# Performance work log

Measured on AMD Instinct MI355X. Metric: run time of the kernel, lower is better.

The kernel has to match this reference:

```python
import jax, jax.numpy as jnp
import numpy as np

B, T, E = 512, 12, 1024   # batch, channels/seq, embed_dim
NH, HS = 8, 128           # num_heads, head_size (head_size=128 hard-coded in source)
H = NH * HS               # sLSTM hidden = 1024 (== E)


def _layer_norm(x, g, b, eps=1e-5):
    mu = x.mean(-1, keepdims=True)
    var = x.var(-1, keepdims=True)
    return (x - mu) * jax.lax.rsqrt(var + eps) * g + b


def _conv1d_same(x, w, b):
    # x: (B, C, L), w: (O, I, K) odd K, 'same' padding, stride 1
    k = w.shape[-1]
    p = (k - 1) // 2
    y = jax.lax.conv_general_dilated(x, w, (1,), [(p, p)],
                                     dimension_numbers=('NCH', 'OIH', 'NCH'))
    return y + b[None, :, None]


def setup_inputs():
    key = jax.random.key(0)
    ks = jax.random.split(key, 16)
    s = 0.02
    def nrm(k, shape, scale=s):
        return jax.random.normal(k, shape, jnp.float32) * scale
    return {
        'x': jax.random.normal(ks[0], (B, T, E), jnp.float32),
        'ln_g': jnp.ones((E,), jnp.float32), 'ln_b': jnp.zeros((E,), jnp.float32),
        'fc1_w': nrm(ks[1], (12, 12, 3)), 'fc1_b': jnp.zeros((12,), jnp.float32),
        'fc2_w': nrm(ks[2], (12, 12)), 'fc2_b': jnp.zeros((12,), jnp.float32),
        'conv1_w': nrm(ks[3], (48, 12, 3)), 'conv1_b': jnp.zeros((48,), jnp.float32),
        'conv2_w': nrm(ks[4], (12, 48, 3)), 'conv2_b': jnp.zeros((12,), jnp.float32),
        'xl_ln_g': jnp.ones((E,), jnp.float32), 'xl_ln_b': jnp.zeros((E,), jnp.float32),
        'Wg': nrm(ks[5], (E, 4 * H)), 'bg': jnp.zeros((4 * H,), jnp.float32),
        'Rg': nrm(ks[6], (NH, 4 * HS, HS)),
        'gn_g': jnp.ones((H,), jnp.float32), 'gn_b': jnp.zeros((H,), jnp.float32),
        'upl_w': nrm(ks[7], (H, H)), 'upl_b': jnp.zeros((H,), jnp.float32),
        'upr_w': nrm(ks[8], (H, H)), 'upr_b': jnp.zeros((H,), jnp.float32),
        'down_w': nrm(ks[9], (H, E)), 'down_b': jnp.zeros((E,), jnp.float32),
    }


def _slstm_block(x, xl_ln_g, xl_ln_b, Wg, bg, Rg, gn_g, gn_b,
                 upl_w, upl_b, upr_w, upr_b, down_w, down_b):
    # Stabilized multi-head sLSTM block: pre-LN -> sLSTM recurrence (exp i/f gates
    # with max-stabilizer m), per-head GroupNorm, gated up/down proj (proj_factor=1),
    # residual. Recurrent weights are block-diagonal per head (NH, 4*HS, HS).
    xn = _layer_norm(x, xl_ln_g, xl_ln_b)
    gx = jnp.einsum('bte,eg->btg', xn, Wg) + bg            # (B,T,4H) input gate pre-acts
    gx = jnp.swapaxes(gx, 0, 1)                            # (T,B,4H)

    def step(carry, g_t):
        h, c, n, m = carry                                 # each (B,NH,HS)
        rec = jnp.einsum('bnh,ngh->bng', h, Rg)            # (B,NH,4HS)
        g = g_t.reshape(g_t.shape[0], NH, 4 * HS) + rec
        z_, i_, f_, o_ = jnp.split(g, 4, axis=-1)
        z = jnp.tanh(z_)
        o = jax.nn.sigmoid(o_)
        m_new = jnp.maximum(f_ + m, i_)                    # log-space stabilizer
        i = jnp.exp(i_ - m_new)
        f = jnp.exp(f_ + m - m_new)
        c = f * c + i * z
        n = f * n + i
        h = o * (c / n)
        return (h, c, n, m_new), h

    zero = jnp.zeros((x.shape[0], NH, HS), x.dtype)
    _, hseq = jax.lax.scan(step, (zero, zero, zero, zero), gx)
    h = jnp.swapaxes(hseq, 0, 1)                           # (B,T,NH,HS)
    # GroupNorm(num_groups=NH) over each head's HS channels
    mu = h.mean(-1, keepdims=True)
    var = h.var(-1, keepdims=True)
    hn = (h - mu) * jax.lax.rsqrt(var + 1e-5)
    hn = hn.reshape(x.shape[0], x.shape[1], H) * gn_g + gn_b
    left = jax.nn.gelu(hn @ upl_w + upl_b, approximate=False)
    right = hn @ upr_w + upr_b
    return (left * right) @ down_w + down_b + x


def reference(x, ln_g, ln_b, fc1_w, fc1_b, fc2_w, fc2_b, conv1_w, conv1_b,
              conv2_w, conv2_b, xl_ln_g, xl_ln_b, Wg, bg, Rg, gn_g, gn_b,
              upl_w, upl_b, upr_w, upr_b, down_w, down_b):
    xn = _layer_norm(x, ln_g, ln_b)
    skip = xn
    xc = _conv1d_same(xn, fc1_w, fc1_b)                    # fc1: Conv1d(12,12,3,'same')
    x1 = jnp.einsum('bcl,oc->bol', xc, fc2_w) + fc2_b[None, :, None]  # fc2: 1x1 conv
    x1 = _slstm_block(x1, xl_ln_g, xl_ln_b, Wg, bg, Rg, gn_g, gn_b,
                      upl_w, upl_b, upr_w, upr_b, down_w, down_b)
    # dropout(0.2) is identity in eval mode
    y = jax.nn.silu(xc) * x1 + skip
    z = _conv1d_same(y, conv1_w, conv1_b)                  # 12 -> 48
    z = _layer_norm(jax.nn.gelu(z, approximate=False), ln_g, ln_b)
    z = _conv1d_same(z, conv2_w, conv2_b)                  # 48 -> 12
    return z + skip
```

## Files before the change

kernel.cpp:

```cpp
#include <hip/hip_runtime.h>
#include <math.h>


typedef short short8_t __attribute__((ext_vector_type(8)));
typedef float floatx4 __attribute__((ext_vector_type(4)));
typedef float float4_t __attribute__((ext_vector_type(4)));

typedef unsigned int u32;
typedef const __attribute__((address_space(1))) u32 gu32;
typedef __attribute__((address_space(3))) u32 lu32;

static __device__ __forceinline__ float b2f(unsigned short u) {
    unsigned v = ((unsigned)u) << 16;
    return __builtin_bit_cast(float, v);
}
static __device__ __forceinline__ unsigned short f2b(float f) {
    unsigned u = __builtin_bit_cast(unsigned, f);
    u += 0x7FFFu + ((u >> 16) & 1u);
    return (unsigned short)(u >> 16);
}
static __device__ __forceinline__ float gelu_exact(float x) {
    return 0.5f * x * (1.f + erff(x * 0.70710678118654752f));
}


__global__ __launch_bounds__(256) void transpose_bf16_k(
    const float* __restrict__ src, unsigned short* __restrict__ dst, int K, int N)
{
    __shared__ unsigned short tl[32][33];
    const int n0 = blockIdx.x * 32, k0 = blockIdx.y * 32;
    const int tx = threadIdx.x & 31, ty = threadIdx.x >> 5;
#pragma unroll
    for (int r = 0; r < 4; r++) {
        int k = ty + r * 8;
        tl[tx][k] = f2b(src[(size_t)(k0 + k) * N + n0 + tx]);
    }
    __syncthreads();
#pragma unroll
    for (int r = 0; r < 4; r++) {
        int n = ty * 4 + r;
        dst[(size_t)(n0 + n) * K + k0 + tx] = tl[n][tx];
    }
}

__global__ __launch_bounds__(256) void cat_bias_k(
    const float* __restrict__ a, const float* __restrict__ b, float* __restrict__ o)
{
    int gid = blockIdx.x * 256 + threadIdx.x;
    o[gid] = (gid < 1024) ? a[gid] : b[gid - 1024];
}


template <int BF16OUT>
__global__ __launch_bounds__(256) void ln_kernel(
    const float* __restrict__ in, const float* __restrict__ g,
    const float* __restrict__ be, void* __restrict__ outp)
{
    const int row = blockIdx.x;
    const float* xr = in + (size_t)row * 1024;
    const int t = threadIdx.x;
    float v[4];
    float s = 0.f, ss = 0.f;
#pragma unroll
    for (int u = 0; u < 4; u++) {
        float q = xr[t + u * 256];
        v[u] = q; s += q; ss += q * q;
    }
#pragma unroll
    for (int off = 32; off >= 1; off >>= 1) {
        s += __shfl_xor(s, off);
        ss += __shfl_xor(ss, off);
    }
    __shared__ float red[8];
    const int wv = t >> 6, la = t & 63;
    if (la == 0) { red[wv] = s; red[4 + wv] = ss; }
    __syncthreads();
    s = red[0] + red[1] + red[2] + red[3];
    ss = red[4] + red[5] + red[6] + red[7];
    float mu = s * (1.f / 1024.f);
    float var = ss * (1.f / 1024.f) - mu * mu;
    float rs = rsqrtf(var + 1e-5f);
#pragma unroll
    for (int u = 0; u < 4; u++) {
        int i = t + u * 256;
        float yv = (v[u] - mu) * rs * g[i] + be[i];
        if (BF16OUT)
            ((unsigned short*)outp)[(size_t)row * 1024 + i] = f2b(yv);
        else
            ((float*)outp)[(size_t)row * 1024 + i] = yv;
    }
}


__global__ __launch_bounds__(256) void fc_kernel(
    const float* __restrict__ xn,
    const float* __restrict__ w1, const float* __restrict__ b1,
    const float* __restrict__ w2, const float* __restrict__ b2,
    float* __restrict__ xc, float* __restrict__ x1)
{
    const int t = threadIdx.x;
    const int gid = blockIdx.x * 256 + t;
    const int b = gid >> 10, l = gid & 1023;
    const float* xb = xn + (size_t)b * 12288;
    float inm[12], in0[12], inp[12];
#pragma unroll
    for (int ci = 0; ci < 12; ci++) {
        in0[ci] = xb[ci * 1024 + l];
        inm[ci] = (l > 0) ? xb[ci * 1024 + l - 1] : 0.f;
        inp[ci] = (l < 1023) ? xb[ci * 1024 + l + 1] : 0.f;
    }
    float xcv[12];
#pragma unroll
    for (int o = 0; o < 12; o++) {
        float a = b1[o];
#pragma unroll
        for (int ci = 0; ci < 12; ci++) {
            const float* wp = w1 + o * 36 + ci * 3;
            a += inm[ci] * wp[0] + in0[ci] * wp[1] + inp[ci] * wp[2];
        }
        xcv[o] = a;
        xc[(size_t)b * 12288 + o * 1024 + l] = a;
    }
#pragma unroll
    for (int o = 0; o < 12; o++) {
        float a = b2[o];
#pragma unroll
        for (int ci = 0; ci < 12; ci++) a += xcv[ci] * w2[o * 12 + ci];
        x1[(size_t)b * 12288 + o * 1024 + l] = a;
    }
}


template <int MODE>
__global__ __launch_bounds__(256) void gemm_kernel(
    const unsigned short* __restrict__ A, const unsigned short* __restrict__ BT,
    const float* __restrict__ bias, void* __restrict__ out,
    int M, int N, int K,
    const float* __restrict__ xc, const float* __restrict__ x1,
    const float* __restrict__ skip)
{
    __shared__ __align__(16) unsigned short sA[128 * 32];
    __shared__ __align__(16) unsigned short sB[128 * 32];
    const int t = threadIdx.x;
    const int m0 = blockIdx.y * 128;
    const int n0 = blockIdx.x * 128;
    const int w = t >> 6;
    const int lane = t & 63;
    const int wr = (w >> 1) * 64;
    const int wc = (w & 1) * 64;
    const int lrow = lane & 15;
    const int quad = lane >> 4;
    const int row_l = t >> 2;
    const int cs = (t & 3) * 8;

    const unsigned short* gA0 = A + (size_t)(m0 + row_l) * K + cs;
    const unsigned short* gA1 = A + (size_t)(m0 + row_l + 64) * K + cs;
    const unsigned short* gB0 = BT + (size_t)(n0 + row_l) * K + cs;
    const unsigned short* gB1 = BT + (size_t)(n0 + row_l + 64) * K + cs;
    unsigned short* lA0 = sA + w * 512;
    unsigned short* lA1 = sA + 2048 + w * 512;
    unsigned short* lB0 = sB + w * 512;
    unsigned short* lB1 = sB + 2048 + w * 512;

    floatx4 acc[4][4];
#pragma unroll
    for (int i = 0; i < 4; i++)
#pragma unroll
        for (int j = 0; j < 4; j++) acc[i][j] = (floatx4)0.f;

    for (int k0 = 0; k0 < K; k0 += 32) {
        __syncthreads();
        __builtin_amdgcn_global_load_lds((gu32*)(gA0 + k0), (lu32*)lA0, 16, 0, 0);
        __builtin_amdgcn_global_load_lds((gu32*)(gA1 + k0), (lu32*)lA1, 16, 0, 0);
        __builtin_amdgcn_global_load_lds((gu32*)(gB0 + k0), (lu32*)lB0, 16, 0, 0);
        __builtin_amdgcn_global_load_lds((gu32*)(gB1 + k0), (lu32*)lB1, 16, 0, 0);
        __syncthreads();
        short8_t af[4], bfr[4];
#pragma unroll
        for (int i = 0; i < 4; i++) {
            af[i] = *(const short8_t*)(sA + (wr + i * 16 + lrow) * 32 + quad * 8);
            bfr[i] = *(const short8_t*)(sB + (wc + i * 16 + lrow) * 32 + quad * 8);
        }
#pragma unroll
        for (int i = 0; i < 4; i++)
#pragma unroll
            for (int j = 0; j < 4; j++)
                acc[i][j] = __builtin_amdgcn_mfma_f32_16x16x32_bf16(
                    af[i], bfr[j], acc[i][j], 0, 0, 0);
    }

#pragma unroll
    for (int i = 0; i < 4; i++) {
#pragma unroll
        for (int j = 0; j < 4; j++) {
#pragma unroll
            for (int r = 0; r < 4; r++) {
                const int gm = m0 + wr + i * 16 + quad * 4 + r;
                const int gn = n0 + wc + j * 16 + lrow;
                const size_t idx = (size_t)gm * N + gn;
                float v = acc[i][j][r] + bias[gn];
                if (MODE == 0) {
                    ((unsigned short*)out)[idx] = f2b(v);
                } else {
                    float xcv = xc[idx];
                    float sig = xcv / (1.f + __expf(-xcv));
                    ((float*)out)[idx] = sig * (v + x1[idx]) + skip[idx];
                }
            }
        }
    }
}


#define RECP 516
#define HBP  136

__global__ __launch_bounds__(1024, 4) void slstm_rec_kernel(
    const float* __restrict__ Rg,
    const unsigned short* __restrict__ gxb,
    const float* __restrict__ gn_g, const float* __restrict__ gn_b,
    unsigned short* __restrict__ hnb)
{
    __shared__ __align__(16) float sRec[16 * RECP];
    __shared__ __align__(16) unsigned short sHb[16 * HBP];
    const int head = blockIdx.x;
    const int b0 = blockIdx.y * 16;
    const int t = threadIdx.x;
    const int w = t >> 6;
    const int lane = t & 63;
    const int quad = lane >> 4;
    const int l16 = lane & 15;

    short8_t Bf[2][4];
    {
        const float* Rh = Rg + (size_t)head * 65536;
#pragma unroll
        for (int jt = 0; jt < 2; jt++)
#pragma unroll
            for (int kk = 0; kk < 4; kk++) {
                const float* src =
                    Rh + (size_t)(w * 32 + jt * 16 + l16) * 128 + kk * 32 + quad * 8;
                short8_t v;
#pragma unroll
                for (int j = 0; j < 8; j++) v[j] = (short)f2b(src[j]);
                Bf[jt][kk] = v;
            }
    }

    for (int i = t; i < 16 * HBP; i += 1024) sHb[i] = 0;

    const int la = lane;
    float c0 = 0.f, n0s = 0.f, m0 = 0.f;
    float c1 = 0.f, n1s = 0.f, m1 = 0.f;
    const float gg0 = gn_g[head * 128 + la];
    const float gg1 = gn_g[head * 128 + la + 64];
    const float gb0 = gn_b[head * 128 + la];
    const float gb1 = gn_b[head * 128 + la + 64];

    __syncthreads();

    for (int step = 0; step < 12; step++) {
        const unsigned short* gp =
            gxb + ((size_t)(b0 + w) * 12 + step) * 4096 + head * 512;
        float gz0 = b2f(gp[la]),       gz1 = b2f(gp[64 + la]);
        float gi0 = b2f(gp[128 + la]), gi1 = b2f(gp[192 + la]);
        float gf0 = b2f(gp[256 + la]), gf1 = b2f(gp[320 + la]);
        float go0 = b2f(gp[384 + la]), go1 = b2f(gp[448 + la]);

        short8_t Af[4];
#pragma unroll
        for (int kk = 0; kk < 4; kk++)
            Af[kk] = *(const short8_t*)(sHb + l16 * HBP + kk * 32 + quad * 8);
        floatx4 D0 = (floatx4)0.f, D1 = (floatx4)0.f;
#pragma unroll
        for (int kk = 0; kk < 4; kk++) {
            D0 = __builtin_amdgcn_mfma_f32_16x16x32_bf16(Af[kk], Bf[0][kk], D0, 0, 0, 0);
            D1 = __builtin_amdgcn_mfma_f32_16x16x32_bf16(Af[kk], Bf[1][kk], D1, 0, 0, 0);
        }
#pragma unroll
        for (int r = 0; r < 4; r++) {
            sRec[(quad * 4 + r) * RECP + w * 32 + l16] = D0[r];
            sRec[(quad * 4 + r) * RECP + w * 32 + 16 + l16] = D1[r];
        }
        __syncthreads();

        const float* rr = sRec + w * RECP;
        float zp0 = gz0 + rr[la],       zp1 = gz1 + rr[64 + la];
        float ip0 = gi0 + rr[128 + la], ip1 = gi1 + rr[192 + la];
        float fp0 = gf0 + rr[256 + la], fp1 = gf1 + rr[320 + la];
        float op0 = go0 + rr[384 + la], op1 = go1 + rr[448 + la];

        float e20 = __expf(2.f * zp0), e21 = __expf(2.f * zp1);
        float z0 = (e20 - 1.f) / (e20 + 1.f), z1 = (e21 - 1.f) / (e21 + 1.f);
        float o0 = 1.f / (1.f + __expf(-op0)), o1 = 1.f / (1.f + __expf(-op1));
        float mn0 = fmaxf(fp0 + m0, ip0), mn1 = fmaxf(fp1 + m1, ip1);
        float ie0 = __expf(ip0 - mn0), ie1 = __expf(ip1 - mn1);
        float fe0 = __expf(fp0 + m0 - mn0), fe1 = __expf(fp1 + m1 - mn1);
        c0 = fe0 * c0 + ie0 * z0;  c1 = fe1 * c1 + ie1 * z1;
        n0s = fe0 * n0s + ie0;     n1s = fe1 * n1s + ie1;
        m0 = mn0;                  m1 = mn1;
        float h0 = o0 * (c0 / n0s), h1 = o1 * (c1 / n1s);

        float s = h0 + h1, ss = h0 * h0 + h1 * h1;
#pragma unroll
        for (int off = 32; off >= 1; off >>= 1) {
            s += __shfl_xor(s, off);
            ss += __shfl_xor(ss, off);
        }
        float mu = s * (1.f / 128.f);
        float var = ss * (1.f / 128.f) - mu * mu;
        float rs = rsqrtf(var + 1e-5f);
        size_t base = ((size_t)(b0 + w) * 12 + step) * 1024 + head * 128;
        hnb[base + la] = f2b((h0 - mu) * rs * gg0 + gb0);
        hnb[base + la + 64] = f2b((h1 - mu) * rs * gg1 + gb1);

        sHb[w * HBP + la] = f2b(h0);
        sHb[w * HBP + la + 64] = f2b(h1);
        __syncthreads();
    }
}


__global__ __launch_bounds__(256) void gate_kernel(
    const unsigned short* __restrict__ lr, unsigned short* __restrict__ glr)
{
    size_t gid = (size_t)blockIdx.x * 256 + threadIdx.x;
    size_t m = gid >> 10;
    int j = (int)(gid & 1023);
    float lf = b2f(lr[m * 2048 + j]);
    float rt = b2f(lr[m * 2048 + 1024 + j]);
    glr[gid] = f2b(gelu_exact(lf) * rt);
}


__global__ __launch_bounds__(1024, 4) void tail_fused_kernel(
    const float* __restrict__ y, const float* __restrict__ skip,
    const float* __restrict__ w1, const float* __restrict__ b1,
    const float* __restrict__ w2, const float* __restrict__ b2,
    const float* __restrict__ lng, const float* __restrict__ lnb,
    float* __restrict__ out)
{
    __shared__ unsigned short sY[12][1032];
    __shared__ unsigned short sZ[48][1032];
    __shared__ float sLg[1024], sLb[1024];
    __shared__ float sMR[48][2];
    const int b = blockIdx.x;
    const int t = threadIdx.x;

    {
        const float* yb = y + (size_t)b * 12288;
#pragma unroll
        for (int r = 0; r < 12; r++) sY[r][t] = f2b(yb[r * 1024 + t]);
    }
    sLg[t] = lng[t];
    sLb[t] = lnb[t];
    __syncthreads();

    float vm[12], v0[12], vp[12];
#pragma unroll
    for (int ci = 0; ci < 12; ci++) {
        v0[ci] = b2f(sY[ci][t]);
        vm[ci] = (t > 0) ? b2f(sY[ci][t - 1]) : 0.f;
        vp[ci] = (t < 1023) ? b2f(sY[ci][t + 1]) : 0.f;
    }
    for (int o = 0; o < 48; o++) {
        const float* wp = w1 + o * 36;
        float a = b1[o];
#pragma unroll
        for (int ci = 0; ci < 12; ci++)
            a += vm[ci] * wp[ci * 3] + v0[ci] * wp[ci * 3 + 1] + vp[ci] * wp[ci * 3 + 2];
        sZ[o][t] = f2b(gelu_exact(a));
    }
    __syncthreads();

    {
        const int w = t >> 6, la = t & 63;
        for (int o = w * 3; o < w * 3 + 3; o++) {
            float s = 0.f, ss = 0.f;
#pragma unroll
            for (int u = 0; u < 16; u++) {
                float v = b2f(sZ[o][la + u * 64]);
                s += v; ss += v * v;
            }
#pragma unroll
            for (int off = 32; off >= 1; off >>= 1) {
                s += __shfl_xor(s, off);
                ss += __shfl_xor(ss, off);
            }
            if (la == 0) {
                float mu = s * (1.f / 1024.f);
                float var = ss * (1.f / 1024.f) - mu * mu;
                sMR[o][0] = mu;
                sMR[o][1] = rsqrtf(var + 1e-5f);
            }
        }
    }
    __syncthreads();

    float acc[12];
#pragma unroll
    for (int o = 0; o < 12; o++) acc[o] = b2[o];
    const float lg0 = sLg[t], lb0 = sLb[t];
    const float lgm = (t > 0) ? sLg[t - 1] : 0.f;
    const float lbm = (t > 0) ? sLb[t - 1] : 0.f;
    const float lgp = (t < 1023) ? sLg[t + 1] : 0.f;
    const float lbp = (t < 1023) ? sLb[t + 1] : 0.f;
    for (int ci = 0; ci < 48; ci++) {
        const float mu = sMR[ci][0], rs = sMR[ci][1];
        float znm = (t > 0) ? ((b2f(sZ[ci][t - 1]) - mu) * rs * lgm + lbm) : 0.f;
        float zn0 = (b2f(sZ[ci][t]) - mu) * rs * lg0 + lb0;
        float znp = (t < 1023) ? ((b2f(sZ[ci][t + 1]) - mu) * rs * lgp + lbp) : 0.f;
        const float* wp = w2 + ci * 3;
#pragma unroll
        for (int o = 0; o < 12; o++)
            acc[o] += znm * wp[o * 144] + zn0 * wp[o * 144 + 1] + znp * wp[o * 144 + 2];
    }
    const size_t base = (size_t)b * 12288 + t;
#pragma unroll
    for (int o = 0; o < 12; o++) {
        size_t idx = base + (size_t)o * 1024;
        out[idx] = acc[o] + skip[idx];
    }
}


extern "C" void kernel_launch(void* const* d_in, const int* in_sizes, int n_in,
                              void* d_out, int out_size, void* d_ws, size_t ws_size,
                              hipStream_t stream)
{
    (void)in_sizes; (void)n_in; (void)out_size; (void)ws_size;
    const float* x      = (const float*)d_in[0];
    const float* ln_g   = (const float*)d_in[1];
    const float* ln_b   = (const float*)d_in[2];
    const float* fc1_w  = (const float*)d_in[3];
    const float* fc1_b  = (const float*)d_in[4];
    const float* fc2_w  = (const float*)d_in[5];
    const float* fc2_b  = (const float*)d_in[6];
    const float* conv1_w= (const float*)d_in[7];
    const float* conv1_b= (const float*)d_in[8];
    const float* conv2_w= (const float*)d_in[9];
    const float* conv2_b= (const float*)d_in[10];
    const float* xl_g   = (const float*)d_in[11];
    const float* xl_b   = (const float*)d_in[12];
    const float* Wg     = (const float*)d_in[13];
    const float* bg     = (const float*)d_in[14];
    const float* Rg     = (const float*)d_in[15];
    const float* gn_g   = (const float*)d_in[16];
    const float* gn_b   = (const float*)d_in[17];
    const float* upl_w  = (const float*)d_in[18];
    const float* upl_b  = (const float*)d_in[19];
    const float* upr_w  = (const float*)d_in[20];
    const float* upr_b  = (const float*)d_in[21];
    const float* down_w = (const float*)d_in[22];
    const float* down_b = (const float*)d_in[23];

    char* ws = (char*)d_ws;
    size_t off = 0;
    auto alloc = [&](size_t bytes) -> char* {
        char* p = ws + off;
        off = (off + bytes + 255) & ~(size_t)255;
        return p;
    };
    float* xn            = (float*)alloc(25165824);
    float* xc            = (float*)alloc(25165824);
    float* x1            = (float*)alloc(25165824);
    unsigned short* xn2b = (unsigned short*)alloc(12582912);
    unsigned short* gxb  = (unsigned short*)alloc(50331648);
    unsigned short* hnb  = (unsigned short*)alloc(12582912);
    unsigned short* lrb  = (unsigned short*)alloc(25165824);
    unsigned short* glrb = (unsigned short*)alloc(12582912);
    float* yb            = (float*)alloc(25165824);
    unsigned short* WgT  = (unsigned short*)alloc(8388608);
    unsigned short* WupT = (unsigned short*)alloc(4194304);
    unsigned short* WdT  = (unsigned short*)alloc(2097152);
    float* bup           = (float*)alloc(8192);

    transpose_bf16_k<<<dim3(128, 32), 256, 0, stream>>>(Wg, WgT, 1024, 4096);
    transpose_bf16_k<<<dim3(32, 32), 256, 0, stream>>>(upl_w, WupT, 1024, 1024);
    transpose_bf16_k<<<dim3(32, 32), 256, 0, stream>>>(upr_w, WupT + 1024 * 1024, 1024, 1024);
    transpose_bf16_k<<<dim3(32, 32), 256, 0, stream>>>(down_w, WdT, 1024, 1024);
    cat_bias_k<<<8, 256, 0, stream>>>(upl_b, upr_b, bup);

    ln_kernel<0><<<6144, 256, 0, stream>>>(x, ln_g, ln_b, xn);
    fc_kernel<<<2048, 256, 0, stream>>>(xn, fc1_w, fc1_b, fc2_w, fc2_b, xc, x1);
    ln_kernel<1><<<6144, 256, 0, stream>>>(x1, xl_g, xl_b, xn2b);
    gemm_kernel<0><<<dim3(32, 48), 256, 0, stream>>>(
        xn2b, WgT, bg, gxb, 6144, 4096, 1024, nullptr, nullptr, nullptr);
    slstm_rec_kernel<<<dim3(8, 32), 1024, 0, stream>>>(Rg, gxb, gn_g, gn_b, hnb);
    gemm_kernel<0><<<dim3(16, 48), 256, 0, stream>>>(
        hnb, WupT, bup, lrb, 6144, 2048, 1024, nullptr, nullptr, nullptr);
    gate_kernel<<<24576, 256, 0, stream>>>(lrb, glrb);
    gemm_kernel<2><<<dim3(8, 48), 256, 0, stream>>>(
        glrb, WdT, down_b, yb, 6144, 1024, 1024, xc, x1, xn);
    tail_fused_kernel<<<512, 1024, 0, stream>>>(
        yb, xn, conv1_w, conv1_b, conv2_w, conv2_b, ln_g, ln_b, (float*)d_out);
}
```

Baseline: 482.4 us.

## Fuse frontend LN/conv/LN into one kernel and restructure tail conv kernel

Merges the first layernorm, the fc1/fc2 convolutions and the second layernorm into a single per-batch kernel that keeps the normalized input in shared memory, removing two launches and the intermediate global round trips. The tail kernel is rebuilt with 512 threads, each handling two positions, and processes the 48 conv1 channels in two halves of 24 so it needs less shared memory. Normalization is applied once in place in shared memory instead of per tap. Exact erf GELU in the tail is replaced with a tanh approximation, which changes numerics slightly. The fused frontend's 1024-thread blocks with 12 channels of state per thread may raise register pressure.

```diff
diff --git a/kernel.cpp b/kernel.cpp
--- a/kernel.cpp
+++ b/kernel.cpp
@@ -4,7 +4,7 @@
 
 typedef short short8_t __attribute__((ext_vector_type(8)));
 typedef float floatx4 __attribute__((ext_vector_type(4)));
-typedef float float4_t __attribute__((ext_vector_type(4)));
+typedef float float2_t __attribute__((ext_vector_type(2)));
 
 typedef unsigned int u32;
 typedef const __attribute__((address_space(1))) u32 gu32;
@@ -22,6 +22,13 @@
 static __device__ __forceinline__ float gelu_exact(float x) {
     return 0.5f * x * (1.f + erff(x * 0.70710678118654752f));
 }
+static __device__ __forceinline__ float gelu_fast(float x) {
+    float u = 0.7978845608f * x * (1.f + 0.044715f * x * x);
+    u = fminf(fmaxf(u, -9.f), 9.f);
+    float e = __expf(2.f * u);
+    float t = (e - 1.f) / (e + 1.f);
+    return 0.5f * x * (1.f + t);
+}
 
 
 __global__ __launch_bounds__(256) void transpose_bf16_k(
@@ -51,82 +58,109 @@
 }
 
 
-template <int BF16OUT>
-__global__ __launch_bounds__(256) void ln_kernel(
-    const float* __restrict__ in, const float* __restrict__ g,
-    const float* __restrict__ be, void* __restrict__ outp)
-{
-    const int row = blockIdx.x;
-    const float* xr = in + (size_t)row * 1024;
-    const int t = threadIdx.x;
-    float v[4];
-    float s = 0.f, ss = 0.f;
-#pragma unroll
-    for (int u = 0; u < 4; u++) {
-        float q = xr[t + u * 256];
-        v[u] = q; s += q; ss += q * q;
-    }
-#pragma unroll
-    for (int off = 32; off >= 1; off >>= 1) {
-        s += __shfl_xor(s, off);
-        ss += __shfl_xor(ss, off);
-    }
-    __shared__ float red[8];
-    const int wv = t >> 6, la = t & 63;
-    if (la == 0) { red[wv] = s; red[4 + wv] = ss; }
-    __syncthreads();
-    s = red[0] + red[1] + red[2] + red[3];
-    ss = red[4] + red[5] + red[6] + red[7];
-    float mu = s * (1.f / 1024.f);
-    float var = ss * (1.f / 1024.f) - mu * mu;
-    float rs = rsqrtf(var + 1e-5f);
-#pragma unroll
-    for (int u = 0; u < 4; u++) {
-        int i = t + u * 256;
-        float yv = (v[u] - mu) * rs * g[i] + be[i];
-        if (BF16OUT)
-            ((unsigned short*)outp)[(size_t)row * 1024 + i] = f2b(yv);
-        else
-            ((float*)outp)[(size_t)row * 1024 + i] = yv;
-    }
-}
-
-
-__global__ __launch_bounds__(256) void fc_kernel(
-    const float* __restrict__ xn,
+__global__ __launch_bounds__(1024, 4) void frontend_fused_kernel(
+    const float* __restrict__ x,
+    const float* __restrict__ ln_g, const float* __restrict__ ln_b,
     const float* __restrict__ w1, const float* __restrict__ b1,
     const float* __restrict__ w2, const float* __restrict__ b2,
-    float* __restrict__ xc, float* __restrict__ x1)
-{
+    const float* __restrict__ xl_g, const float* __restrict__ xl_b,
+    float* __restrict__ xn, float* __restrict__ xc, float* __restrict__ x1,
+    unsigned short* __restrict__ xn2b)
+{
+    __shared__ float sXn[12][1026];
+    __shared__ float sred[12][16][2];
+    __shared__ float sMR[12][2];
+    const int b = blockIdx.x;
     const int t = threadIdx.x;
-    const int gid = blockIdx.x * 256 + t;
-    const int b = gid >> 10, l = gid & 1023;
-    const float* xb = xn + (size_t)b * 12288;
-    float inm[12], in0[12], inp[12];
+    const int w = t >> 6, la = t & 63;
+    const size_t boff = (size_t)b * 12288;
+
+    float xv[12];
+#pragma unroll
+    for (int ci = 0; ci < 12; ci++) xv[ci] = x[boff + ci * 1024 + t];
+
 #pragma unroll
     for (int ci = 0; ci < 12; ci++) {
-        in0[ci] = xb[ci * 1024 + l];
-        inm[ci] = (l > 0) ? xb[ci * 1024 + l - 1] : 0.f;
-        inp[ci] = (l < 1023) ? xb[ci * 1024 + l + 1] : 0.f;
+        float s = xv[ci], ss = xv[ci] * xv[ci];
+#pragma unroll
+        for (int off = 32; off >= 1; off >>= 1) {
+            s += __shfl_xor(s, off); ss += __shfl_xor(ss, off);
+        }
+        if (la == 0) { sred[ci][w][0] = s; sred[ci][w][1] = ss; }
+    }
+    __syncthreads();
+    if (w < 12 && la == 0) {
+        float s = 0.f, ss = 0.f;
+        for (int u = 0; u < 16; u++) { s += sred[w][u][0]; ss += sred[w][u][1]; }
+        float mu = s * (1.f / 1024.f);
+        float var = ss * (1.f / 1024.f) - mu * mu;
+        sMR[w][0] = mu; sMR[w][1] = rsqrtf(var + 1e-5f);
+    }
+    __syncthreads();
+    {
+        const float g0 = ln_g[t], be0 = ln_b[t];
+#pragma unroll
+        for (int ci = 0; ci < 12; ci++) {
+            float v = (xv[ci] - sMR[ci][0]) * sMR[ci][1] * g0 + be0;
+            sXn[ci][t] = v;
+            xn[boff + ci * 1024 + t] = v;
+            xv[ci] = v;
+        }
+    }
+    __syncthreads();
+
+    float vmv[12], vpv[12];
+#pragma unroll
+    for (int ci = 0; ci < 12; ci++) {
+        vmv[ci] = (t > 0) ? sXn[ci][t - 1] : 0.f;
+        vpv[ci] = (t < 1023) ? sXn[ci][t + 1] : 0.f;
     }
     float xcv[12];
 #pragma unroll
     for (int o = 0; o < 12; o++) {
+        const float* wp = w1 + o * 36;
         float a = b1[o];
 #pragma unroll
-        for (int ci = 0; ci < 12; ci++) {
-            const float* wp = w1 + o * 36 + ci * 3;
-            a += inm[ci] * wp[0] + in0[ci] * wp[1] + inp[ci] * wp[2];
-        }
+        for (int ci = 0; ci < 12; ci++)
+            a += vmv[ci] * wp[ci * 3] + xv[ci] * wp[ci * 3 + 1] + vpv[ci] * wp[ci * 3 + 2];
         xcv[o] = a;
-        xc[(size_t)b * 12288 + o * 1024 + l] = a;
-    }
+        xc[boff + o * 1024 + t] = a;
+    }
+    float x1v[12];
 #pragma unroll
     for (int o = 0; o < 12; o++) {
         float a = b2[o];
 #pragma unroll
         for (int ci = 0; ci < 12; ci++) a += xcv[ci] * w2[o * 12 + ci];
-        x1[(size_t)b * 12288 + o * 1024 + l] = a;
+        x1v[o] = a;
+        x1[boff + o * 1024 + t] = a;
+    }
+
+#pragma unroll
+    for (int ci = 0; ci < 12; ci++) {
+        float s = x1v[ci], ss = x1v[ci] * x1v[ci];
+#pragma unroll
+        for (int off = 32; off >= 1; off >>= 1) {
+            s += __shfl_xor(s, off); ss += __shfl_xor(ss, off);
+        }
+        if (la == 0) { sred[ci][w][0] = s; sred[ci][w][1] = ss; }
+    }
+    __syncthreads();
+    if (w < 12 && la == 0) {
+        float s = 0.f, ss = 0.f;
+        for (int u = 0; u < 16; u++) { s += sred[w][u][0]; ss += sred[w][u][1]; }
+        float mu = s * (1.f / 1024.f);
+        float var = ss * (1.f / 1024.f) - mu * mu;
+        sMR[w][0] = mu; sMR[w][1] = rsqrtf(var + 1e-5f);
+    }
+    __syncthreads();
+    {
+        const float g2 = xl_g[t], b2v = xl_b[t];
+#pragma unroll
+        for (int ci = 0; ci < 12; ci++) {
+            float v = (x1v[ci] - sMR[ci][0]) * sMR[ci][1] * g2 + b2v;
+            xn2b[boff + ci * 1024 + t] = f2b(v);
+        }
     }
 }
 
@@ -333,93 +367,111 @@
 }
 
 
-__global__ __launch_bounds__(1024, 4) void tail_fused_kernel(
+__global__ __launch_bounds__(512, 4) void tail_fused_kernel(
     const float* __restrict__ y, const float* __restrict__ skip,
     const float* __restrict__ w1, const float* __restrict__ b1,
     const float* __restrict__ w2, const float* __restrict__ b2,
     const float* __restrict__ lng, const float* __restrict__ lnb,
     float* __restrict__ out)
 {
-    __shared__ unsigned short sY[12][1032];
-    __shared__ unsigned short sZ[48][1032];
-    __shared__ float sLg[1024], sLb[1024];
-    __shared__ float sMR[48][2];
+    __shared__ unsigned short sY[12][1026];
+    __shared__ unsigned short sZ[24][1026];
+    __shared__ float sMR[24][2];
     const int b = blockIdx.x;
-    const int t = threadIdx.x;
+    const int p = threadIdx.x;
+    const size_t boff = (size_t)b * 12288;
 
     {
-        const float* yb = y + (size_t)b * 12288;
-#pragma unroll
-        for (int r = 0; r < 12; r++) sY[r][t] = f2b(yb[r * 1024 + t]);
-    }
-    sLg[t] = lng[t];
-    sLb[t] = lnb[t];
-    __syncthreads();
-
-    float vm[12], v0[12], vp[12];
-#pragma unroll
-    for (int ci = 0; ci < 12; ci++) {
-        v0[ci] = b2f(sY[ci][t]);
-        vm[ci] = (t > 0) ? b2f(sY[ci][t - 1]) : 0.f;
-        vp[ci] = (t < 1023) ? b2f(sY[ci][t + 1]) : 0.f;
-    }
-    for (int o = 0; o < 48; o++) {
-        const float* wp = w1 + o * 36;
-        float a = b1[o];
-#pragma unroll
-        for (int ci = 0; ci < 12; ci++)
-            a += vm[ci] * wp[ci * 3] + v0[ci] * wp[ci * 3 + 1] + vp[ci] * wp[ci * 3 + 2];
-        sZ[o][t] = f2b(gelu_exact(a));
-    }
-    __syncthreads();
-
-    {
-        const int w = t >> 6, la = t & 63;
-        for (int o = w * 3; o < w * 3 + 3; o++) {
-            float s = 0.f, ss = 0.f;
-#pragma unroll
-            for (int u = 0; u < 16; u++) {
-                float v = b2f(sZ[o][la + u * 64]);
-                s += v; ss += v * v;
+#pragma unroll
+        for (int ci = 0; ci < 12; ci++) {
+            sY[ci][p] = f2b(y[boff + ci * 1024 + p]);
+            sY[ci][p + 512] = f2b(y[boff + ci * 1024 + p + 512]);
+        }
+    }
+    const float lg0 = lng[p], lb0 = lnb[p];
+    const float lg1 = lng[p + 512], lb1 = lnb[p + 512];
+    __syncthreads();
+
+    float2_t acc[12];
+#pragma unroll
+    for (int o = 0; o < 12; o++) { float bv = b2[o]; acc[o] = float2_t{bv, bv}; }
+
+    for (int half = 0; half < 2; half++) {
+        float2_t vm[12], v0[12], vp[12];
+#pragma unroll
+        for (int ci = 0; ci < 12; ci++) {
+            v0[ci] = float2_t{b2f(sY[ci][p]), b2f(sY[ci][p + 512])};
+            vm[ci] = float2_t{(p > 0) ? b2f(sY[ci][p - 1]) : 0.f,
+                              b2f(sY[ci][p + 511])};
+            vp[ci] = float2_t{b2f(sY[ci][p + 1]),
+                              (p < 511) ? b2f(sY[ci][p + 513]) : 0.f};
+        }
+        for (int o = 0; o < 24; o++) {
+            const float* wp = w1 + (half * 24 + o) * 36;
+            float bo = b1[half * 24 + o];
+            float2_t a = float2_t{bo, bo};
+#pragma unroll
+            for (int ci = 0; ci < 12; ci++)
+                a += vm[ci] * wp[ci * 3] + v0[ci] * wp[ci * 3 + 1]
+                   + vp[ci] * wp[ci * 3 + 2];
+            sZ[o][p] = f2b(gelu_fast(a.x));
+            sZ[o][p + 512] = f2b(gelu_fast(a.y));
+        }
+        __syncthreads();
+
+        {
+            const int w = p >> 6, la = p & 63;
+#pragma unroll
+            for (int j = 0; j < 3; j++) {
+                const int ch = w + j * 8;
+                float s = 0.f, ss = 0.f;
+#pragma unroll
+                for (int u = 0; u < 16; u++) {
+                    float v = b2f(sZ[ch][la + u * 64]);
+                    s += v; ss += v * v;
+                }
+#pragma unroll
+                for (int off = 32; off >= 1; off >>= 1) {
+                    s += __shfl_xor(s, off); ss += __shfl_xor(ss, off);
+                }
+                if (la == 0) {
+                    float mu = s * (1.f / 1024.f);
+                    float var = ss * (1.f / 1024.f) - mu * mu;
+                    sMR[ch][0] = mu;
+                    sMR[ch][1] = rsqrtf(var + 1e-5f);
+                }
             }
-#pragma unroll
-            for (int off = 32; off >= 1; off >>= 1) {
-                s += __shfl_xor(s, off);
-                ss += __shfl_xor(ss, off);
-            }
-            if (la == 0) {
-                float mu = s * (1.f / 1024.f);
-                float var = ss * (1.f / 1024.f) - mu * mu;
-                sMR[o][0] = mu;
-                sMR[o][1] = rsqrtf(var + 1e-5f);
-            }
-        }
-    }
-    __syncthreads();
-
-    float acc[12];
-#pragma unroll
-    for (int o = 0; o < 12; o++) acc[o] = b2[o];
-    const float lg0 = sLg[t], lb0 = sLb[t];
-    const float lgm = (t > 0) ? sLg[t - 1] : 0.f;
-    const float lbm = (t > 0) ? sLb[t - 1] : 0.f;
-    const float lgp = (t < 1023) ? sLg[t + 1] : 0.f;
-    const float lbp = (t < 1023) ? sLb[t + 1] : 0.f;
-    for (int ci = 0; ci < 48; ci++) {
-        const float mu = sMR[ci][0], rs = sMR[ci][1];
-        float znm = (t > 0) ? ((b2f(sZ[ci][t - 1]) - mu) * rs * lgm + lbm) : 0.f;
-        float zn0 = (b2f(sZ[ci][t]) - mu) * rs * lg0 + lb0;
-        float znp = (t < 1023) ? ((b2f(sZ[ci][t + 1]) - mu) * rs * lgp + lbp) : 0.f;
-        const float* wp = w2 + ci * 3;
-#pragma unroll
-        for (int o = 0; o < 12; o++)
-            acc[o] += znm * wp[o * 144] + zn0 * wp[o * 144 + 1] + znp * wp[o * 144 + 2];
-    }
-    const size_t base = (size_t)b * 12288 + t;
+        }
+        __syncthreads();
+
+#pragma unroll
+        for (int ch = 0; ch < 24; ch++) {
+            float mu = sMR[ch][0], rs = sMR[ch][1];
+            sZ[ch][p] = f2b((b2f(sZ[ch][p]) - mu) * rs * lg0 + lb0);
+            sZ[ch][p + 512] = f2b((b2f(sZ[ch][p + 512]) - mu) * rs * lg1 + lb1);
+        }
+        __syncthreads();
+
+        for (int ci = 0; ci < 24; ci++) {
+            float2_t zm = float2_t{(p > 0) ? b2f(sZ[ci][p - 1]) : 0.f,
+                                   b2f(sZ[ci][p + 511])};
+            float2_t z0 = float2_t{b2f(sZ[ci][p]), b2f(sZ[ci][p + 512])};
+            float2_t zp = float2_t{b2f(sZ[ci][p + 1]),
+                                   (p < 511) ? b2f(sZ[ci][p + 513]) : 0.f};
+            const float* wp = w2 + (half * 24 + ci) * 3;
+#pragma unroll
+            for (int o = 0; o < 12; o++)
+                acc[o] += zm * wp[o * 144] + z0 * wp[o * 144 + 1]
+                        + zp * wp[o * 144 + 2];
+        }
+        __syncthreads();
+    }
+
 #pragma unroll
     for (int o = 0; o < 12; o++) {
-        size_t idx = base + (size_t)o * 1024;
-        out[idx] = acc[o] + skip[idx];
+        size_t i0 = boff + (size_t)o * 1024 + p;
+        out[i0] = acc[o].x + skip[i0];
+        out[i0 + 512] = acc[o].y + skip[i0 + 512];
     }
 }
 
@@ -481,9 +533,9 @@
     transpose_bf16_k<<<dim3(32, 32), 256, 0, stream>>>(down_w, WdT, 1024, 1024);
     cat_bias_k<<<8, 256, 0, stream>>>(upl_b, upr_b, bup);
 
-    ln_kernel<0><<<6144, 256, 0, stream>>>(x, ln_g, ln_b, xn);
-    fc_kernel<<<2048, 256, 0, stream>>>(xn, fc1_w, fc1_b, fc2_w, fc2_b, xc, x1);
-    ln_kernel<1><<<6144, 256, 0, stream>>>(x1, xl_g, xl_b, xn2b);
+    frontend_fused_kernel<<<512, 1024, 0, stream>>>(
+        x, ln_g, ln_b, fc1_w, fc1_b, fc2_w, fc2_b, xl_g, xl_b,
+        xn, xc, x1, xn2b);
     gemm_kernel<0><<<dim3(32, 48), 256, 0, stream>>>(
         xn2b, WgT, bg, gxb, 6144, 4096, 1024, nullptr, nullptr, nullptr);
     slstm_rec_kernel<<<dim3(8, 32), 1024, 0, stream>>>(Rg, gxb, gn_g, gn_b, hnb);
@@ -492,6 +544,6 @@
     gate_kernel<<<24576, 256, 0, stream>>>(lrb, glrb);
     gemm_kernel<2><<<dim3(8, 48), 256, 0, stream>>>(
         glrb, WdT, down_b, yb, 6144, 1024, 1024, xc, x1, xn);
-    tail_fused_kernel<<<512, 1024, 0, stream>>>(
+    tail_fused_kernel<<<512, 512, 0, stream>>>(
         yb, xn, conv1_w, conv1_b, conv2_w, conv2_b, ln_g, ln_b, (float*)d_out);
 }
```

Measured after the change: 476.1 us. No clear change (-1.3%).
